# Optimization experiments

Hardware: AMD Instinct MI355X
Metric: run time of the kernel (lower is better)

## Reference

```python
import jax, jax.numpy as jnp
import numpy as np

B, S, D, DV, DO, H = 4, 2048, 1024, 1024, 1024, 16
DH = D // H  # key depth per head


def setup_inputs() -> dict:
    key = jax.random.key(0)
    k1, k2, k3, k4, k5, k6, k7 = jax.random.split(key, 7)
    return {
        "query_antecedent": jax.random.normal(k1, (B, S, D), dtype=jnp.float32),
        "memory_antecedent": jax.random.normal(k2, (B, S, D), dtype=jnp.float32),
        "bias": jax.random.normal(k3, (B, S, S), dtype=jnp.float32),
        # weight-init uniform(-0.1, 0.1) as in the torch Linear helper; stored [in, out]
        "Wq": jax.random.uniform(k4, (D, D), minval=-0.1, maxval=0.1, dtype=jnp.float32),
        "Wk": jax.random.uniform(k5, (D, D), minval=-0.1, maxval=0.1, dtype=jnp.float32),
        "Wv": jax.random.uniform(k6, (DV, DV), minval=-0.1, maxval=0.1, dtype=jnp.float32),
        "Wo": jax.random.uniform(k7, (DV, DO), minval=-0.1, maxval=0.1, dtype=jnp.float32),
    }


def reference(query_antecedent, memory_antecedent, bias, Wq, Wk, Wv, Wo):
    scale = DH ** -0.5
    q = (query_antecedent @ Wq) * scale            # [B,S,D]
    k = memory_antecedent @ Wk                      # [B,S,D]
    v = memory_antecedent @ Wv                      # [B,S,DV]
    # split heads: [B,S,H,DH]
    q = q.reshape(B, S, H, DH)
    k = k.reshape(B, S, H, DH)
    v = v.reshape(B, S, H, DV // H)
    logits = jnp.einsum("bshd,bthd->bhst", q, k) + bias[:, None, :, :]  # [B,H,S,S]
    weights = jax.nn.softmax(logits, axis=-1)
    out = jnp.einsum("bhst,bthd->bshd", weights, v)  # [B,S,H,DH]
    out = out.reshape(B, S, DV)
    return out @ Wo
```

## Files before the change

kernel.cpp:

```cpp
#include <hip/hip_runtime.h>
#include <hip/hip_bf16.h>

#define BB 4
#define SS 2048
#define DD 1024
#define HH 16
#define DHH 64

typedef __attribute__((ext_vector_type(8))) short short8;
typedef __attribute__((ext_vector_type(4))) float floatx4;
typedef __attribute__((ext_vector_type(16))) float floatx16;
typedef __attribute__((ext_vector_type(4))) int int4v;

__device__ inline short f2bf(float x) {
  union { float f; unsigned u; } v; v.f = x;
  unsigned r = v.u + 0x7FFFu + ((v.u >> 16) & 1u);
  return (short)(r >> 16);
}
__device__ inline float bf2f(short x) {
  union { unsigned u; float f; } v;
  v.u = ((unsigned)(unsigned short)x) << 16;
  return v.f;
}
__device__ inline int cvtpk(float lo, float hi) {
  int r;
  asm("v_cvt_pk_bf16_f32 %0, %1, %2" : "=v"(r) : "v"(lo), "v"(hi));
  return r;
}
__device__ inline void pl32swap(int& a, int& b) {
  asm("v_permlane32_swap_b32 %0, %1" : "+v"(a), "+v"(b));
}

typedef __attribute__((address_space(1))) const unsigned int GUI;
typedef __attribute__((address_space(3))) unsigned int LUI;
__device__ inline void gload16(const void* g, void* l) {
  __builtin_amdgcn_global_load_lds((GUI*)g, (LUI*)l, 16, 0, 0);
}

__global__ __launch_bounds__(256) void cvt2_kernel(const float* __restrict__ in0,
                                                   const float* __restrict__ in1,
                                                   short* __restrict__ out, int n4half) {
  int i = blockIdx.x * 256 + threadIdx.x;
  if (i >= 2 * n4half) return;
  const float* src = (i < n4half) ? in0 : in1;
  int j = (i < n4half) ? i : i - n4half;
  float4 v = ((const float4*)src)[j];
  short4 o;
  o.x = f2bf(v.x); o.y = f2bf(v.y); o.z = f2bf(v.z); o.w = f2bf(v.w);
  ((short4*)out)[i] = o;
}

__global__ __launch_bounds__(256) void wtrans4_kernel(const float* __restrict__ W0,
                                                      const float* __restrict__ W1,
                                                      const float* __restrict__ W2,
                                                      const float* __restrict__ W3,
                                                      short* __restrict__ o0,
                                                      short* __restrict__ o1,
                                                      short* __restrict__ o2,
                                                      short* __restrict__ o3,
                                                      float s0) {
  __shared__ float tile[16][17];
  const int z = blockIdx.z;
  const float* in = (z == 0) ? W0 : (z == 1) ? W1 : (z == 2) ? W2 : W3;
  short* out = (z == 0) ? o0 : (z == 1) ? o1 : (z == 2) ? o2 : o3;
  const float scale = (z == 0) ? s0 : 1.0f;
  int tx = threadIdx.x & 15, ty = threadIdx.x >> 4;
  int k = blockIdx.y * 16 + ty;
  int n = blockIdx.x * 16 + tx;
  tile[ty][tx] = in[(size_t)k * 1024 + n];
  __syncthreads();
  int n2 = blockIdx.x * 16 + ty;
  int k2 = blockIdx.y * 16 + tx;
  out[(size_t)n2 * 1024 + k2] = f2bf(tile[tx][ty] * scale);
}

__global__ __launch_bounds__(256) void btrans_blk(const float* __restrict__ in,
                                                  short* __restrict__ out, float scale) {
  __shared__ short tile[64][68];
  const int t = threadIdx.x;
  const int b = blockIdx.z;
  const int q0 = blockIdx.x * 64, kv0 = blockIdx.y * 64;
  const float* gin = in + ((size_t)b * SS + q0) * SS + kv0;
#pragma unroll
  for (int i = 0; i < 4; ++i) {
    int idx = t + 256 * i;
    int row = idx >> 4, c4 = idx & 15;
    float4 v = ((const float4*)(gin + (size_t)row * SS))[c4];
    tile[row][c4 * 4 + 0] = f2bf(v.x * scale);
    tile[row][c4 * 4 + 1] = f2bf(v.y * scale);
    tile[row][c4 * 4 + 2] = f2bf(v.z * scale);
    tile[row][c4 * 4 + 3] = f2bf(v.w * scale);
  }
  __syncthreads();
  short* gout = out + (size_t)((b * 32 + (kv0 >> 6)) * 16) * 8192 + (size_t)q0 * 4;
#pragma unroll
  for (int i = 0; i < 4; ++i) {
    int idx = t + 256 * i;
    int s = idx >> 6, ql = idx & 63;
    int kvt = s >> 3, g = (s >> 1) & 3, hi = s & 1;
    short4 v = *(const short4*)&tile[ql][kvt * 32 + g * 8 + hi * 4];
    *(short4*)&gout[(size_t)s * 8192 + (size_t)ql * 4] = v;
  }
}

__global__ __launch_bounds__(256) void vtrans_kernel(const short* __restrict__ in,
                                                     short* __restrict__ out, int ldin) {
  __shared__ int tile[64][33];
  const int t = threadIdx.x;
  const int b = blockIdx.z;
  const int s0 = blockIdx.x * 64, d0 = blockIdx.y * 64;
  const int* gin = (const int*)(in + (size_t)b * SS * ldin);
  const int ldi2 = ldin >> 1;
  int* gout = (int*)(out + (size_t)b * DD * SS);
#pragma unroll
  for (int i = 0; i < 8; ++i) {
    int idx = t + i * 256;
    int row = idx >> 5, col = idx & 31;
    tile[row][col] = gin[(size_t)(s0 + row) * ldi2 + (d0 >> 1) + col];
  }
  __syncthreads();
#pragma unroll
  for (int i = 0; i < 8; ++i) {
    int idx = t + i * 256;
    int d = idx >> 5, spc = idx & 31;
    int a = tile[2 * spc][d >> 1];
    int c = tile[2 * spc + 1][d >> 1];
    int o = (d & 1) ? (((a >> 16) & 0xffff) | (c & 0xffff0000))
                    : ((a & 0xffff) | (c << 16));
    gout[(size_t)(d0 + d) * (SS / 2) + (s0 >> 1) + spc] = o;
  }
}

template<int OUT_F32, int TM>
__global__ __launch_bounds__(256) void gemm_kernel(const short* __restrict__ A,
                                                   const short* __restrict__ Bt,
                                                   void* __restrict__ Cout,
                                                   int M, int N, int K) {
  constexpr int MI = TM / 32;
  __shared__ alignas(16) short As[2][TM][32];
  __shared__ alignas(16) short Bs[2][128][32];
  const int t = threadIdx.x;
  const int lane = t & 63, wave = t >> 6;
  const int wr = wave >> 1, wc = wave & 1;
  const int l15 = lane & 15, l4 = lane >> 4;

  const int hw = blockIdx.x;
  const int L = (hw & 7) * ((int)gridDim.x >> 3) + (hw >> 3);
  const int NY = N >> 7;
  const int bxm = L / NY, byn = L % NY;

  floatx4 acc[MI][4];
#pragma unroll
  for (int i = 0; i < MI; ++i)
#pragma unroll
    for (int j = 0; j < 4; ++j) acc[i][j] = (floatx4){0.f, 0.f, 0.f, 0.f};

  const short* Ag = A + (size_t)bxm * TM * K;
  const short* Bg = Bt + (size_t)byn * 128 * K;
  const int o0 = t * 16, o1 = t * 16 + 4096;
  const int r0 = o0 >> 6, r1 = o1 >> 6;
  const int c0 = (((o0 >> 1) & 31) ^ ((r0 & 3) << 3));
  const int c1 = (((o1 >> 1) & 31) ^ ((r1 & 3) << 3));
  const int rbase = wr * (TM / 2) + l15;
  const int cbase = wc * 64 + l15;
  const int koff = (l4 ^ (l15 & 3)) * 8;

#define GSTAGE(buf, k0)                                                    \
  {                                                                        \
    gload16(&Ag[(size_t)r0 * K + (k0) + c0], (char*)As[buf] + o0);         \
    if (TM == 128)                                                         \
      gload16(&Ag[(size_t)r1 * K + (k0) + c1], (char*)As[buf] + o1);       \
    gload16(&Bg[(size_t)r0 * K + (k0) + c0], (char*)Bs[buf] + o0);         \
    gload16(&Bg[(size_t)r1 * K + (k0) + c1], (char*)Bs[buf] + o1);         \
  }

  GSTAGE(0, 0)
  __syncthreads();
  int cur = 0;
  for (int k0 = 0; k0 < K; k0 += 32) {
    if (k0 + 32 < K) { GSTAGE(cur ^ 1, k0 + 32) }
    short8 af[MI], bfr[4];
#pragma unroll
    for (int mi = 0; mi < MI; ++mi) af[mi] = *(const short8*)&As[cur][rbase + mi * 16][koff];
#pragma unroll
    for (int ni = 0; ni < 4; ++ni) bfr[ni] = *(const short8*)&Bs[cur][cbase + ni * 16][koff];
    __builtin_amdgcn_s_setprio(1);
#pragma unroll
    for (int mi = 0; mi < MI; ++mi)
#pragma unroll
      for (int ni = 0; ni < 4; ++ni)
        acc[mi][ni] = __builtin_amdgcn_mfma_f32_16x16x32_bf16(af[mi], bfr[ni], acc[mi][ni], 0, 0, 0);
    __builtin_amdgcn_s_setprio(0);
    __syncthreads();
    cur ^= 1;
  }
#undef GSTAGE

  const int row0 = bxm * TM + wr * (TM / 2) + l4 * 4;
  const int col0 = byn * 128 + wc * 64 + l15;
  if (OUT_F32) {
    float* Cf = (float*)Cout;
#pragma unroll
    for (int mi = 0; mi < MI; ++mi)
#pragma unroll
      for (int ni = 0; ni < 4; ++ni)
#pragma unroll
        for (int r = 0; r < 4; ++r)
          Cf[(size_t)(row0 + mi * 16 + r) * N + col0 + ni * 16] = acc[mi][ni][r];
  } else {
    short* Cs = (short*)Cout;
#pragma unroll
    for (int mi = 0; mi < MI; ++mi)
#pragma unroll
      for (int ni = 0; ni < 4; ++ni)
#pragma unroll
        for (int r = 0; r < 4; ++r)
          Cs[(size_t)(row0 + mi * 16 + r) * N + col0 + ni * 16] = f2bf(acc[mi][ni][r]);
  }
}

__global__ __launch_bounds__(256, 4) void attn_kernel(const short* __restrict__ Q,
                                                      const short* __restrict__ K,
                                                      const short* __restrict__ VT,
                                                      const short* __restrict__ bias_blk,
                                                      short* __restrict__ O, int ldk) {
  __shared__ alignas(16) short Klds[2][64][64];
  __shared__ alignas(16) short Vtl[2][64][64];

  const int t = threadIdx.x;
  const int lane = t & 63, wave = t >> 6;
  const int hw = blockIdx.x;
  const int L = (hw & 7) * 128 + (hw >> 3);
  const int bh = L >> 4;
  const int q0 = (L & 15) * 128;
  const int b = bh >> 4, h = bh & 15;
  const int l31 = lane & 31, hi = lane >> 5;

  const short* Qb = Q + (size_t)b * SS * DD + h * DHH;
  const short* Kb = K + (size_t)b * SS * ldk + h * DHH;
  const short* VTb = VT + ((size_t)b * DD + h * DHH) * SS;
  const short* Bl = bias_blk + (size_t)(b * 32 * 16) * 8192 + (size_t)hi * 8192
                    + (size_t)(q0 + wave * 32 + l31) * 4;

  const int sr0 = t >> 3;
  const int scb = ((t & 7) ^ (sr0 & 7)) * 8;

#define STAGE_KV(buf, kvb)                                                              \
  {                                                                                     \
    gload16(&Kb[(size_t)((kvb) + sr0) * ldk + scb], (char*)&Klds[buf][0][0] + t * 16);  \
    gload16(&Kb[(size_t)((kvb) + sr0 + 32) * ldk + scb],                                \
            (char*)&Klds[buf][0][0] + 4096 + t * 16);                                   \
    gload16(&VTb[(size_t)sr0 * SS + (kvb) + scb], (char*)&Vtl[buf][0][0] + t * 16);     \
    gload16(&VTb[(size_t)(sr0 + 32) * SS + (kvb) + scb],                                \
            (char*)&Vtl[buf][0][0] + 4096 + t * 16);                                    \
  }
#define BIAS_PREF(kvb)                                                                  \
  {                                                                                     \
    int kt16 = ((kvb) >> 6) << 4;                                                       \
    _Pragma("unroll")                                                                   \
    for (int kvt = 0; kvt < 2; ++kvt)                                                   \
      _Pragma("unroll")                                                                 \
      for (int g = 0; g < 4; ++g)                                                       \
        br[kvt * 4 + g] = *(const short4*)&Bl[(size_t)(kt16 + kvt * 8 + g * 2) * 8192]; \
  }

  short4 br[8];
  STAGE_KV(0, 0)
  BIAS_PREF(0)

  const int q = wave * 32 + l31;
  short8 qf[4];
  {
    int qrow = q0 + q;
#pragma unroll
    for (int dc = 0; dc < 4; ++dc)
      qf[dc] = *(const short8*)&Qb[(size_t)qrow * DD + dc * 16 + hi * 8];
  }

  floatx16 acc_pv[2];
#pragma unroll
  for (int r = 0; r < 16; ++r) { acc_pv[0][r] = 0.f; acc_pv[1][r] = 0.f; }
  float psum = 0.f;

  __syncthreads();
  int cur = 0;
  for (int kv0 = 0; kv0 < SS; kv0 += 64) {
    if (kv0 + 64 < SS) STAGE_KV(cur ^ 1, kv0 + 64)

#pragma unroll
    for (int kvt = 0; kvt < 2; ++kvt) {
      floatx16 c_;
#pragma unroll
      for (int g = 0; g < 4; ++g) {
        short4 b4 = br[kvt * 4 + g];
        c_[4 * g + 0] = bf2f(b4.x); c_[4 * g + 1] = bf2f(b4.y);
        c_[4 * g + 2] = bf2f(b4.z); c_[4 * g + 3] = bf2f(b4.w);
      }
      int kr = kvt * 32 + l31;
      __builtin_amdgcn_s_setprio(1);
#pragma unroll
      for (int dc = 0; dc < 4; ++dc) {
        short8 kf = *(const short8*)&Klds[cur][kr][((2 * dc + hi) ^ (kr & 7)) * 8];
        c_ = __builtin_amdgcn_mfma_f32_32x32x16_bf16(kf, qf[dc], c_, 0, 0, 0);
      }
      __builtin_amdgcn_s_setprio(0);

      if (kvt == 1 && kv0 + 64 < SS) BIAS_PREF(kv0 + 64)

      int dd[8];
#pragma unroll
      for (int i = 0; i < 8; ++i) {
        float e0 = __builtin_amdgcn_exp2f(c_[2 * i]);
        float e1 = __builtin_amdgcn_exp2f(c_[2 * i + 1]);
        psum += e0 + e1;
        dd[i] = cvtpk(e0, e1);
      }

#pragma unroll
      for (int ks2 = 0; ks2 < 2; ++ks2) {
        int a0 = dd[4 * ks2 + 0], a1 = dd[4 * ks2 + 1];
        int a2 = dd[4 * ks2 + 2], a3 = dd[4 * ks2 + 3];
        pl32swap(a0, a2);
        pl32swap(a1, a3);
        int4v w; w[0] = a0; w[1] = a1; w[2] = a2; w[3] = a3;
        short8 pf = *(short8*)&w;
        int ks = kvt * 2 + ks2;
        __builtin_amdgcn_s_setprio(1);
#pragma unroll
        for (int dt = 0; dt < 2; ++dt) {
          int vr = dt * 32 + l31;
          short8 vf = *(const short8*)&Vtl[cur][vr][((2 * ks + hi) ^ (vr & 7)) * 8];
          acc_pv[dt] = __builtin_amdgcn_mfma_f32_32x32x16_bf16(vf, pf, acc_pv[dt], 0, 0, 0);
        }
        __builtin_amdgcn_s_setprio(0);
      }
    }
    __syncthreads();
    cur ^= 1;
  }
#undef STAGE_KV
#undef BIAS_PREF

  float ssum = psum + __shfl_xor(psum, 32);
  float inv = 1.0f / ssum;

  short* ep = (short*)Klds + wave * 2048;
#pragma unroll
  for (int dt = 0; dt < 2; ++dt)
#pragma unroll
    for (int r = 0; r < 16; ++r) {
      int d = dt * 32 + (r & 3) + 8 * (r >> 2) + 4 * hi;
      int chunk = d >> 3, doff = d & 7;
      ep[l31 * 64 + ((chunk ^ (l31 & 7)) << 3) + doff] = f2bf(acc_pv[dt][r] * inv);
    }
  short* Ob = O + (size_t)b * SS * DD + h * DHH;
  const int rr = lane >> 3, cc = lane & 7;
#pragma unroll
  for (int ii = 0; ii < 4; ++ii) {
    int q2 = ii * 8 + rr;
    short8 vv = *(const short8*)&ep[q2 * 64 + ((cc ^ (q2 & 7)) << 3)];
    *(short8*)&Ob[(size_t)(q0 + wave * 32 + q2) * DD + cc * 8] = vv;
  }
}

extern "C" void kernel_launch(void* const* d_in, const int* in_sizes, int n_in,
                              void* d_out, int out_size, void* d_ws, size_t ws_size,
                              hipStream_t stream) {
  const float* qa   = (const float*)d_in[0];
  const float* ma   = (const float*)d_in[1];
  const float* bias = (const float*)d_in[2];
  const float* Wq   = (const float*)d_in[3];
  const float* Wk   = (const float*)d_in[4];
  const float* Wv   = (const float*)d_in[5];
  const float* Wo   = (const float*)d_in[6];
  float* out = (float*)d_out;

  char* ws = (char*)d_ws;
  size_t off = 0;
  auto alloc = [&](size_t bytes) {
    char* p = ws + off;
    off += (bytes + 255) & ~(size_t)255;
    return p;
  };
  const size_t nQKV = (size_t)BB * SS * DD;
  short* qa_bf   = (short*)alloc(nQKV * 2);
  short* ma_bf   = (short*)alloc(nQKV * 2);
  short* bias_bk = (short*)alloc((size_t)BB * SS * SS * 2);
  short* Wqt  = (short*)alloc((size_t)DD * DD * 2);
  short* Wkvt = (short*)alloc((size_t)2 * DD * DD * 2);
  short* Wot  = (short*)alloc((size_t)DD * DD * 2);
  short* Qp   = (short*)alloc(nQKV * 2);
  short* KVp  = (short*)alloc(nQKV * 2 * 2);
  short* AOp  = (short*)alloc(nQKV * 2);
  short* VTp  = qa_bf;

  const float LOG2E = 1.4426950408889634f;
  int n4a = (int)(nQKV / 4);
  cvt2_kernel<<<(2 * n4a + 255) / 256, 256, 0, stream>>>(qa, ma, qa_bf, n4a);

  btrans_blk<<<dim3(SS / 64, SS / 64, BB), 256, 0, stream>>>(bias, bias_bk, LOG2E);

  wtrans4_kernel<<<dim3(64, 64, 4), 256, 0, stream>>>(
      Wq, Wk, Wv, Wo, Wqt, Wkvt, Wkvt + (size_t)DD * DD, Wot, 0.125f * LOG2E);

  gemm_kernel<0, 64><<<BB * SS / 64 * (DD / 128), 256, 0, stream>>>(qa_bf, Wqt, Qp, BB * SS, DD, DD);
  gemm_kernel<0, 128><<<BB * SS / 128 * (2 * DD / 128), 256, 0, stream>>>(ma_bf, Wkvt, KVp, BB * SS, 2 * DD, DD);

  vtrans_kernel<<<dim3(SS / 64, DD / 64, BB), 256, 0, stream>>>(KVp + DD, VTp, 2 * DD);

  attn_kernel<<<BB * HH * (SS / 128), 256, 0, stream>>>(Qp, KVp, VTp, bias_bk, AOp, 2 * DD);

  gemm_kernel<1, 64><<<BB * SS / 64 * (DD / 128), 256, 0, stream>>>(AOp, Wot, out, BB * SS, DD, DD);
}
```

Baseline: 264.8 us.

## Fuse V transpose into KV GEMM epilogue and merge prep kernels

The three input-preparation kernels (activation bf16 conversion, weight transpose, bias blocking) are merged into a single launch that dispatches on block index. The K/V projection moves to a dedicated GEMM whose V-half tiles are transposed through swizzled shared memory and written straight into the VT layout. This removes the separate vtrans pass and the intermediate interleaved KV buffer, saving a full read and write of V plus several launches. In exchange, the V-half blocks do extra LDS work and an extra barrier in their epilogue.

```diff
diff --git a/kernel.cpp b/kernel.cpp
--- a/kernel.cpp
+++ b/kernel.cpp
@@ -37,97 +37,70 @@
   __builtin_amdgcn_global_load_lds((GUI*)g, (LUI*)l, 16, 0, 0);
 }
 
-__global__ __launch_bounds__(256) void cvt2_kernel(const float* __restrict__ in0,
-                                                   const float* __restrict__ in1,
-                                                   short* __restrict__ out, int n4half) {
-  int i = blockIdx.x * 256 + threadIdx.x;
-  if (i >= 2 * n4half) return;
-  const float* src = (i < n4half) ? in0 : in1;
-  int j = (i < n4half) ? i : i - n4half;
-  float4 v = ((const float4*)src)[j];
-  short4 o;
-  o.x = f2bf(v.x); o.y = f2bf(v.y); o.z = f2bf(v.z); o.w = f2bf(v.w);
-  ((short4*)out)[i] = o;
-}
-
-__global__ __launch_bounds__(256) void wtrans4_kernel(const float* __restrict__ W0,
-                                                      const float* __restrict__ W1,
-                                                      const float* __restrict__ W2,
-                                                      const float* __restrict__ W3,
-                                                      short* __restrict__ o0,
-                                                      short* __restrict__ o1,
-                                                      short* __restrict__ o2,
-                                                      short* __restrict__ o3,
-                                                      float s0) {
-  __shared__ float tile[16][17];
-  const int z = blockIdx.z;
-  const float* in = (z == 0) ? W0 : (z == 1) ? W1 : (z == 2) ? W2 : W3;
-  short* out = (z == 0) ? o0 : (z == 1) ? o1 : (z == 2) ? o2 : o3;
-  const float scale = (z == 0) ? s0 : 1.0f;
-  int tx = threadIdx.x & 15, ty = threadIdx.x >> 4;
-  int k = blockIdx.y * 16 + ty;
-  int n = blockIdx.x * 16 + tx;
-  tile[ty][tx] = in[(size_t)k * 1024 + n];
-  __syncthreads();
-  int n2 = blockIdx.x * 16 + ty;
-  int k2 = blockIdx.y * 16 + tx;
-  out[(size_t)n2 * 1024 + k2] = f2bf(tile[tx][ty] * scale);
-}
-
-__global__ __launch_bounds__(256) void btrans_blk(const float* __restrict__ in,
-                                                  short* __restrict__ out, float scale) {
-  __shared__ short tile[64][68];
+__global__ __launch_bounds__(256) void prep_kernel(
+    const float* __restrict__ qa, const float* __restrict__ ma,
+    const float* __restrict__ bias,
+    const float* __restrict__ W0, const float* __restrict__ W1,
+    const float* __restrict__ W2, const float* __restrict__ W3,
+    short* __restrict__ qm_bf, short* __restrict__ bias_bk,
+    short* __restrict__ Wqt, short* __restrict__ Wkvt, short* __restrict__ Wot,
+    float wqscale, float bscale) {
+  __shared__ alignas(16) char smemraw[8704];
+  const int blk = blockIdx.x;
   const int t = threadIdx.x;
-  const int b = blockIdx.z;
-  const int q0 = blockIdx.x * 64, kv0 = blockIdx.y * 64;
-  const float* gin = in + ((size_t)b * SS + q0) * SS + kv0;
-#pragma unroll
-  for (int i = 0; i < 4; ++i) {
-    int idx = t + 256 * i;
-    int row = idx >> 4, c4 = idx & 15;
-    float4 v = ((const float4*)(gin + (size_t)row * SS))[c4];
-    tile[row][c4 * 4 + 0] = f2bf(v.x * scale);
-    tile[row][c4 * 4 + 1] = f2bf(v.y * scale);
-    tile[row][c4 * 4 + 2] = f2bf(v.z * scale);
-    tile[row][c4 * 4 + 3] = f2bf(v.w * scale);
-  }
-  __syncthreads();
-  short* gout = out + (size_t)((b * 32 + (kv0 >> 6)) * 16) * 8192 + (size_t)q0 * 4;
-#pragma unroll
-  for (int i = 0; i < 4; ++i) {
-    int idx = t + 256 * i;
-    int s = idx >> 6, ql = idx & 63;
-    int kvt = s >> 3, g = (s >> 1) & 3, hi = s & 1;
-    short4 v = *(const short4*)&tile[ql][kvt * 32 + g * 8 + hi * 4];
-    *(short4*)&gout[(size_t)s * 8192 + (size_t)ql * 4] = v;
-  }
-}
-
-__global__ __launch_bounds__(256) void vtrans_kernel(const short* __restrict__ in,
-                                                     short* __restrict__ out, int ldin) {
-  __shared__ int tile[64][33];
-  const int t = threadIdx.x;
-  const int b = blockIdx.z;
-  const int s0 = blockIdx.x * 64, d0 = blockIdx.y * 64;
-  const int* gin = (const int*)(in + (size_t)b * SS * ldin);
-  const int ldi2 = ldin >> 1;
-  int* gout = (int*)(out + (size_t)b * DD * SS);
-#pragma unroll
-  for (int i = 0; i < 8; ++i) {
-    int idx = t + i * 256;
-    int row = idx >> 5, col = idx & 31;
-    tile[row][col] = gin[(size_t)(s0 + row) * ldi2 + (d0 >> 1) + col];
-  }
-  __syncthreads();
-#pragma unroll
-  for (int i = 0; i < 8; ++i) {
-    int idx = t + i * 256;
-    int d = idx >> 5, spc = idx & 31;
-    int a = tile[2 * spc][d >> 1];
-    int c = tile[2 * spc + 1][d >> 1];
-    int o = (d & 1) ? (((a >> 16) & 0xffff) | (c & 0xffff0000))
-                    : ((a & 0xffff) | (c << 16));
-    gout[(size_t)(d0 + d) * (SS / 2) + (s0 >> 1) + spc] = o;
+  if (blk < 16384) {
+    int i = blk * 256 + t;
+    const int n4half = (BB * SS * DD) / 4;
+    const float* src = (i < n4half) ? qa : ma;
+    int j = (i < n4half) ? i : i - n4half;
+    float4 v = ((const float4*)src)[j];
+    short4 o;
+    o.x = f2bf(v.x); o.y = f2bf(v.y); o.z = f2bf(v.z); o.w = f2bf(v.w);
+    ((short4*)qm_bf)[i] = o;
+  } else if (blk < 32768) {
+    float(*tile)[17] = (float(*)[17])smemraw;
+    int jj = blk - 16384;
+    int z = jj >> 12, rem = jj & 4095;
+    int by = rem >> 6, bx = rem & 63;
+    const float* in = (z == 0) ? W0 : (z == 1) ? W1 : (z == 2) ? W2 : W3;
+    short* out = (z == 0) ? Wqt : (z == 1) ? Wkvt
+                 : (z == 2) ? (Wkvt + (size_t)DD * DD) : Wot;
+    const float scale = (z == 0) ? wqscale : 1.0f;
+    int tx = t & 15, ty = t >> 4;
+    int k = by * 16 + ty;
+    int n = bx * 16 + tx;
+    tile[ty][tx] = in[(size_t)k * 1024 + n];
+    __syncthreads();
+    int n2 = bx * 16 + ty;
+    int k2 = by * 16 + tx;
+    out[(size_t)n2 * 1024 + k2] = f2bf(tile[tx][ty] * scale);
+  } else {
+    short(*tile)[68] = (short(*)[68])smemraw;
+    int jj = blk - 32768;
+    int b = jj >> 10, rem = jj & 1023;
+    int by = rem >> 5, bx = rem & 31;
+    int q0 = bx * 64, kv0 = by * 64;
+    const float* gin = bias + ((size_t)b * SS + q0) * SS + kv0;
+#pragma unroll
+    for (int i = 0; i < 4; ++i) {
+      int idx = t + 256 * i;
+      int row = idx >> 4, c4 = idx & 15;
+      float4 v = ((const float4*)(gin + (size_t)row * SS))[c4];
+      tile[row][c4 * 4 + 0] = f2bf(v.x * bscale);
+      tile[row][c4 * 4 + 1] = f2bf(v.y * bscale);
+      tile[row][c4 * 4 + 2] = f2bf(v.z * bscale);
+      tile[row][c4 * 4 + 3] = f2bf(v.w * bscale);
+    }
+    __syncthreads();
+    short* gout = bias_bk + (size_t)((b * 32 + (kv0 >> 6)) * 16) * 8192 + (size_t)q0 * 4;
+#pragma unroll
+    for (int i = 0; i < 4; ++i) {
+      int idx = t + 256 * i;
+      int s = idx >> 6, ql = idx & 63;
+      int kvt = s >> 3, g = (s >> 1) & 3, hi = s & 1;
+      short4 v = *(const short4*)&tile[ql][kvt * 32 + g * 8 + hi * 4];
+      *(short4*)&gout[(size_t)s * 8192 + (size_t)ql * 4] = v;
+    }
   }
 }
 
@@ -216,6 +189,105 @@
 #pragma unroll
         for (int r = 0; r < 4; ++r)
           Cs[(size_t)(row0 + mi * 16 + r) * N + col0 + ni * 16] = f2bf(acc[mi][ni][r]);
+  }
+}
+
+__global__ __launch_bounds__(256) void gemm_kv(const short* __restrict__ A,
+                                               const short* __restrict__ Bt,
+                                               short* __restrict__ Kp,
+                                               short* __restrict__ VT, int K) {
+  __shared__ alignas(16) short smem[16384];
+  short (*As)[128][32] = (short(*)[128][32])smem;
+  short (*Bs)[128][32] = (short(*)[128][32])(smem + 8192);
+  const int t = threadIdx.x;
+  const int lane = t & 63, wave = t >> 6;
+  const int wr = wave >> 1, wc = wave & 1;
+  const int l15 = lane & 15, l4 = lane >> 4;
+
+  const int hw = blockIdx.x;
+  const int L = (hw & 7) * ((int)gridDim.x >> 3) + (hw >> 3);
+  const int bxm = L >> 4, byn = L & 15;
+
+  floatx4 acc[4][4];
+#pragma unroll
+  for (int i = 0; i < 4; ++i)
+#pragma unroll
+    for (int j = 0; j < 4; ++j) acc[i][j] = (floatx4){0.f, 0.f, 0.f, 0.f};
+
+  const short* Ag = A + (size_t)bxm * 128 * K;
+  const short* Bg = Bt + (size_t)byn * 128 * K;
+  const int o0 = t * 16, o1 = t * 16 + 4096;
+  const int r0 = o0 >> 6, r1 = o1 >> 6;
+  const int c0 = (((o0 >> 1) & 31) ^ ((r0 & 3) << 3));
+  const int c1 = (((o1 >> 1) & 31) ^ ((r1 & 3) << 3));
+  const int rbase = wr * 64 + l15;
+  const int cbase = wc * 64 + l15;
+  const int koff = (l4 ^ (l15 & 3)) * 8;
+
+#define GSTAGE(buf, k0)                                                     \
+  {                                                                         \
+    gload16(&Ag[(size_t)r0 * K + (k0) + c0], (char*)As[buf] + o0);          \
+    gload16(&Ag[(size_t)r1 * K + (k0) + c1], (char*)As[buf] + o1);          \
+    gload16(&Bg[(size_t)r0 * K + (k0) + c0], (char*)Bs[buf] + o0);          \
+    gload16(&Bg[(size_t)r1 * K + (k0) + c1], (char*)Bs[buf] + o1);          \
+  }
+
+  GSTAGE(0, 0)
+  __syncthreads();
+  int cur = 0;
+  for (int k0 = 0; k0 < K; k0 += 32) {
+    if (k0 + 32 < K) { GSTAGE(cur ^ 1, k0 + 32) }
+    short8 af[4], bfr[4];
+#pragma unroll
+    for (int mi = 0; mi < 4; ++mi) af[mi] = *(const short8*)&As[cur][rbase + mi * 16][koff];
+#pragma unroll
+    for (int ni = 0; ni < 4; ++ni) bfr[ni] = *(const short8*)&Bs[cur][cbase + ni * 16][koff];
+    __builtin_amdgcn_s_setprio(1);
+#pragma unroll
+    for (int mi = 0; mi < 4; ++mi)
+#pragma unroll
+      for (int ni = 0; ni < 4; ++ni)
+        acc[mi][ni] = __builtin_amdgcn_mfma_f32_16x16x32_bf16(af[mi], bfr[ni], acc[mi][ni], 0, 0, 0);
+    __builtin_amdgcn_s_setprio(0);
+    __syncthreads();
+    cur ^= 1;
+  }
+#undef GSTAGE
+
+  if (byn < 8) {
+    const int row0 = bxm * 128 + wr * 64 + l4 * 4;
+    const int col0 = byn * 128 + wc * 64 + l15;
+#pragma unroll
+    for (int mi = 0; mi < 4; ++mi)
+#pragma unroll
+      for (int ni = 0; ni < 4; ++ni)
+#pragma unroll
+        for (int r = 0; r < 4; ++r)
+          Kp[(size_t)(row0 + mi * 16 + r) * 1024 + col0 + ni * 16] = f2bf(acc[mi][ni][r]);
+  } else {
+    short* tl = smem;
+#pragma unroll
+    for (int mi = 0; mi < 4; ++mi)
+#pragma unroll
+      for (int ni = 0; ni < 4; ++ni)
+#pragma unroll
+        for (int r = 0; r < 4; ++r) {
+          int srow = wr * 64 + mi * 16 + l4 * 4 + r;
+          int dcol = wc * 64 + ni * 16 + l15;
+          tl[dcol * 128 + (srow ^ ((dcol & 7) << 3))] = f2bf(acc[mi][ni][r]);
+        }
+    __syncthreads();
+    const int b = bxm >> 4;
+    const int s0 = (bxm & 15) * 128;
+    const int d0 = (byn - 8) * 128;
+    short* Vb = VT + ((size_t)b * DD + d0) * SS + s0;
+#pragma unroll
+    for (int i = 0; i < 8; ++i) {
+      int ci = t + 256 * i;
+      int dr = ci >> 4, c = ci & 15;
+      short8 v = *(const short8*)&tl[dr * 128 + ((c ^ (dr & 7)) << 3)];
+      *(short8*)&Vb[(size_t)dr * SS + c * 8] = v;
+    }
   }
 }
 
@@ -390,25 +462,20 @@
   short* Wkvt = (short*)alloc((size_t)2 * DD * DD * 2);
   short* Wot  = (short*)alloc((size_t)DD * DD * 2);
   short* Qp   = (short*)alloc(nQKV * 2);
-  short* KVp  = (short*)alloc(nQKV * 2 * 2);
+  short* Kp   = (short*)alloc(nQKV * 2);
   short* AOp  = (short*)alloc(nQKV * 2);
   short* VTp  = qa_bf;
+  (void)ma_bf;
 
   const float LOG2E = 1.4426950408889634f;
-  int n4a = (int)(nQKV / 4);
-  cvt2_kernel<<<(2 * n4a + 255) / 256, 256, 0, stream>>>(qa, ma, qa_bf, n4a);
-
-  btrans_blk<<<dim3(SS / 64, SS / 64, BB), 256, 0, stream>>>(bias, bias_bk, LOG2E);
-
-  wtrans4_kernel<<<dim3(64, 64, 4), 256, 0, stream>>>(
-      Wq, Wk, Wv, Wo, Wqt, Wkvt, Wkvt + (size_t)DD * DD, Wot, 0.125f * LOG2E);
+  prep_kernel<<<36864, 256, 0, stream>>>(qa, ma, bias, Wq, Wk, Wv, Wo,
+                                         qa_bf, bias_bk, Wqt, Wkvt, Wot,
+                                         0.125f * LOG2E, LOG2E);
 
   gemm_kernel<0, 64><<<BB * SS / 64 * (DD / 128), 256, 0, stream>>>(qa_bf, Wqt, Qp, BB * SS, DD, DD);
-  gemm_kernel<0, 128><<<BB * SS / 128 * (2 * DD / 128), 256, 0, stream>>>(ma_bf, Wkvt, KVp, BB * SS, 2 * DD, DD);
-
-  vtrans_kernel<<<dim3(SS / 64, DD / 64, BB), 256, 0, stream>>>(KVp + DD, VTp, 2 * DD);
-
-  attn_kernel<<<BB * HH * (SS / 128), 256, 0, stream>>>(Qp, KVp, VTp, bias_bk, AOp, 2 * DD);
+  gemm_kv<<<BB * SS / 128 * 16, 256, 0, stream>>>(qa_bf + nQKV, Wkvt, Kp, VTp, DD);
+
+  attn_kernel<<<BB * HH * (SS / 128), 256, 0, stream>>>(Qp, Kp, VTp, bias_bk, AOp, DD);
 
   gemm_kernel<1, 64><<<BB * SS / 64 * (DD / 128), 256, 0, stream>>>(AOp, Wot, out, BB * SS, DD, DD);
 }
```

After: 245.3 us. 7.4% less time.
